# Kernel tuning notes

Measured on AMD Instinct MI355X. Metric: run time of the kernel, lower is better.

The kernel has to match this reference:

```python
import jax, jax.numpy as jnp
import numpy as np

APN, UEN, H, S = 105, 4000, 128, 10
BN_EPS = 1e-5


def _xavier(k, shape):
    fan_out, fan_in = shape
    return jax.random.normal(k, shape, dtype=jnp.float32) * jnp.sqrt(2.0 / (fan_in + fan_out))


def setup_inputs() -> dict:
    key = jax.random.key(0)
    ks = jax.random.split(key, 24)
    inp = {
        "pl": jax.random.normal(ks[0], (APN, UEN), dtype=jnp.float32),
        "require": jax.random.normal(ks[1], (UEN,), dtype=jnp.float32),
        "adj_ue": jax.random.randint(ks[2], (UEN, S), 0, APN, dtype=jnp.int32),
        "adj_ap": jax.random.randint(ks[3], (APN, S), 0, UEN, dtype=jnp.int32),
        # layer-1 Mean_layer weights [embed_dim, feature_dim]
        "W1_ap1": _xavier(ks[4], (H, UEN + APN)),
        "W1_ap2": _xavier(ks[5], (H, 2 * UEN)),
        "W1_ue1": _xavier(ks[6], (H, UEN + APN)),
        "W1_ue2": _xavier(ks[7], (H, 2 * APN)),
        # layer-2 Mean_layer weights
        "W2_ap1": _xavier(ks[8], (H, 4 * H)),
        "W2_ap2": _xavier(ks[9], (H, 4 * H)),
        "W2_ue1": _xavier(ks[10], (H, 4 * H)),
        "W2_ue2": _xavier(ks[11], (H, 4 * H)),
        # heads
        "weight_ap1": _xavier(ks[12], (2 * H, 2 * H)),
        "weight_ap2": _xavier(ks[13], (1, 2 * H)),
        "bais_ap": jax.random.uniform(ks[14], (APN,), dtype=jnp.float32),
        "weight_ue": _xavier(ks[15], (APN, 2 * H)),
        "bais_ue": jax.random.uniform(ks[16], (UEN,), dtype=jnp.float32),
        # BatchNorm1d affine params (training mode, batch stats)
        "bn_gamma": jnp.ones((2 * H,), dtype=jnp.float32),
        "bn_beta": jnp.zeros((2 * H,), dtype=jnp.float32),
    }
    return inp


def _agg(feats, idx):
    # GraphSage mean aggregate, exactly mask.sum/(num_neigh+1) of the original
    g = jnp.take(feats, idx, axis=0)            # [N, S, F]
    return g.sum(axis=1) / (idx.shape[1] + 1.0)  # [N, F]


def _two_hop(one_adj, sec_adj):
    # deterministic stand-in for union(sec_adj over one-hop) + sample(num_sample)
    s = one_adj.shape[1]
    g = jnp.take(sec_adj, one_adj, axis=0)       # [N, S, S]
    d = jnp.arange(s)
    return g[:, d, d]                            # [N, S]


def _layer(W, self_f, other_f, idx):
    comb = jnp.concatenate([self_f, _agg(other_f, idx)], axis=1)  # [N, feat]
    return jax.nn.relu(W @ comb.T)               # [H, N]


def _forward(pl, require, adj_ue, adj_ap, W1_ap1, W1_ap2, W1_ue1, W1_ue2,
             W2_ap1, W2_ap2, W2_ue1, W2_ue2, weight_ap1, weight_ap2,
             bais_ap, weight_ue, bais_ue, bn_gamma, bn_beta):
    feats_ap = pl            # [APN, UEN]
    feats_ue = pl.T          # [UEN, APN]

    ap2ap = _two_hop(adj_ap, adj_ue)   # AP -> AP 2-hop [APN, S]
    ue2ue = _two_hop(adj_ue, adj_ap)   # UE -> UE 2-hop [UEN, S]

    x1 = _layer(W1_ap1, feats_ap, feats_ue, adj_ap)   # [H, APN]
    x2 = _layer(W1_ap2, feats_ap, feats_ap, ap2ap)    # [H, APN]
    x3 = _layer(W1_ue1, feats_ue, feats_ap, adj_ue)   # [H, UEN]
    x4 = _layer(W1_ue2, feats_ue, feats_ue, ue2ue)    # [H, UEN]

    X_ap = jnp.concatenate([x1, x2], axis=0).T        # [APN, 2H]
    X_ue = jnp.concatenate([x3, x4], axis=0).T        # [UEN, 2H]

    x5 = _layer(W2_ap1, X_ap, X_ue, adj_ap)
    x6 = _layer(W2_ap2, X_ap, X_ap, ap2ap)
    x7 = _layer(W2_ue1, X_ue, X_ap, adj_ue)
    x8 = _layer(W2_ue2, X_ue, X_ue, ue2ue)

    X_ap2 = jnp.concatenate([x5, x6], axis=0)         # [2H, APN]
    hidden_pc = weight_ap1 @ X_ap2 + bais_ap          # [2H, APN] + [APN]
    PCoutcome = jax.nn.sigmoid((weight_ap2 @ hidden_pc).T)  # [APN, 1]

    X_ue2 = jnp.concatenate([x7, x8], axis=0)         # [2H, UEN]
    xt = X_ue2.T                                      # [UEN, 2H]
    mean = xt.mean(axis=0)
    var = xt.var(axis=0)                              # biased, training-mode BN
    xbn = ((xt - mean) / jnp.sqrt(var + BN_EPS)) * bn_gamma + bn_beta
    UA = weight_ue @ xbn.T + bais_ue                  # [APN, UEN] + [UEN]

    UA_ori = UA.T                                     # [UEN, APN]
    mx = UA_ori.max(axis=1, keepdims=True)
    mn = UA_ori.min(axis=1, keepdims=True)
    nor = (UA_ori - mx) / (mx - mn)
    UA_de = jax.nn.softmax(nor * 1000.0, axis=1)
    UA_st = jax.nn.softmax(nor, axis=1)
    var_ue = jnp.var(weight_ue, axis=1, ddof=1)       # torch.var unbiased
    return (UA_ori, UA_de, UA_st, PCoutcome, jnp.sum(var_ue))


def reference(pl, require, adj_ue, adj_ap, W1_ap1, W1_ap2, W1_ue1, W1_ue2,
              W2_ap1, W2_ap2, W2_ue1, W2_ue2, weight_ap1, weight_ap2,
              bais_ap, weight_ue, bais_ue, bn_gamma, bn_beta):
    return _forward(pl, require, adj_ue, adj_ap, W1_ap1, W1_ap2, W1_ue1,
                    W1_ue2, W2_ap1, W2_ap2, W2_ue1, W2_ue2, weight_ap1,
                    weight_ap2, bais_ap, weight_ue, bais_ue, bn_gamma, bn_beta)
```

## Files before the change

### kernel.cpp

```cpp
#include <hip/hip_runtime.h>
#include <math.h>
#include <float.h>


#define APN 105
#define UEN 4000
#define H   128
#define H2  256
#define SS  10
#define INV_NEIGH (1.0f/11.0f)
#define NKS 16
#define KSL 250
#define BNB 80

__device__ __forceinline__ float frelu(float v){ return v > 0.f ? v : 0.f; }

__global__ void k_twohop(const int* __restrict__ adj_ue, const int* __restrict__ adj_ap,
                         int* __restrict__ ap2ap, int* __restrict__ ue2ue){
  int idx = blockIdx.x*256 + threadIdx.x;
  if (idx >= (APN+UEN)*SS) return;
  if (idx < APN*SS){
    int s = idx % SS;
    ap2ap[idx] = adj_ue[adj_ap[idx]*SS + s];
  } else {
    int j = idx - APN*SS;
    int s = j % SS;
    ue2ue[j] = adj_ap[adj_ue[j]*SS + s];
  }
}

__device__ __forceinline__ void tile_core(const float (*As)[68], const float (*Bs)[68],
                                          int tx, int ty, float acc[4][4])
{
  #pragma unroll 4
  for (int k=0;k<32;k++){
    float a0 = As[k][ty*4+0], a1 = As[k][ty*4+1];
    float a2 = As[k][ty*4+2], a3 = As[k][ty*4+3];
    float b0 = Bs[k][tx*4+0], b1 = Bs[k][tx*4+1];
    float b2 = Bs[k][tx*4+2], b3 = Bs[k][tx*4+3];
    acc[0][0]=fmaf(a0,b0,acc[0][0]); acc[0][1]=fmaf(a0,b1,acc[0][1]);
    acc[0][2]=fmaf(a0,b2,acc[0][2]); acc[0][3]=fmaf(a0,b3,acc[0][3]);
    acc[1][0]=fmaf(a1,b0,acc[1][0]); acc[1][1]=fmaf(a1,b1,acc[1][1]);
    acc[1][2]=fmaf(a1,b2,acc[1][2]); acc[1][3]=fmaf(a1,b3,acc[1][3]);
    acc[2][0]=fmaf(a2,b0,acc[2][0]); acc[2][1]=fmaf(a2,b1,acc[2][1]);
    acc[2][2]=fmaf(a2,b2,acc[2][2]); acc[2][3]=fmaf(a2,b3,acc[2][3]);
    acc[3][0]=fmaf(a3,b0,acc[3][0]); acc[3][1]=fmaf(a3,b1,acc[3][1]);
    acc[3][2]=fmaf(a3,b2,acc[3][2]); acc[3][3]=fmaf(a3,b3,acc[3][3]);
  }
}

__global__ __launch_bounds__(256) void k_gemA6(
    const float* __restrict__ pl, const float* __restrict__ W1ap1,
    const float* __restrict__ W1ap2, const float* __restrict__ W1ue1,
    float* __restrict__ partial)
{
  __shared__ float As[32][68], Bs[32][68];
  int t = threadIdx.x;
  int n0 = blockIdx.x*64;
  int y = blockIdx.y;
  int ks = blockIdx.z;
  int slice = y>>1, h0 = (y&1)*64, k0 = ks*KSL;
  const float* w; int lda;
  if      (slice == 0){ w = W1ap1;       lda = UEN+APN; }
  else if (slice == 1){ w = W1ap2;       lda = 2*UEN;   }
  else if (slice == 2){ w = W1ap2 + UEN; lda = 2*UEN;   }
  else                { w = W1ue1 + APN; lda = UEN+APN; }
  int tx = t&15, ty = t>>4;
  int hr = t>>2, c0 = (t&3)*8;
  float acc[4][4] = {};
  for (int kc = 0; kc < 256; kc += 32){
    float w8[8], x8[8];
    const float* wr = w + (size_t)(h0+hr)*lda + k0 + kc + c0;
    #pragma unroll
    for (int i=0;i<8;i++) w8[i] = (kc+c0+i < KSL) ? wr[i] : 0.f;
    const float* xr = pl + (size_t)(n0+hr)*UEN + k0 + kc + c0;
    bool nok = (n0+hr < APN);
    #pragma unroll
    for (int i=0;i<8;i++) x8[i] = (nok && kc+c0+i < KSL) ? xr[i] : 0.f;
    __syncthreads();
    #pragma unroll
    for (int i=0;i<8;i++) As[c0+i][hr] = w8[i];
    #pragma unroll
    for (int i=0;i<8;i++) Bs[c0+i][hr] = x8[i];
    __syncthreads();
    tile_core(As, Bs, tx, ty, acc);
  }
  float* po = partial + (size_t)(slice*NKS+ks)*APN*H;
  #pragma unroll
  for (int j=0;j<4;j++){
    int n = n0 + tx*4 + j;
    if (n < APN){
      #pragma unroll
      for (int i=0;i<4;i++) po[(size_t)n*H + h0 + ty*4 + i] = acc[i][j];
    }
  }
}

__global__ __launch_bounds__(256) void k_redA(const float* __restrict__ partial,
                                              float* __restrict__ RA){
  int idx = blockIdx.x*256 + threadIdx.x;
  if (idx >= 4*APN*H) return;
  int slice = idx / (APN*H), r = idx % (APN*H);
  float s = 0.f;
  #pragma unroll
  for (int ks=0;ks<NKS;ks++) s += partial[((size_t)(slice*NKS+ks)*APN*H) + r];
  RA[idx] = s;
}

__global__ __launch_bounds__(256) void k_gemB2(
    const float* __restrict__ pl, const float* __restrict__ W1ap1,
    const float* __restrict__ W1ue1, const float* __restrict__ W1ue2,
    float* __restrict__ T3, float* __restrict__ T4,
    float* __restrict__ U1, float* __restrict__ R4)
{
  __shared__ float As[32][68], Bs[32][68];
  int t = threadIdx.x, u0 = blockIdx.x*64, y = blockIdx.y;
  int z = y>>1, h0 = (y&1)*64;
  const float* w; int lda; float* op;
  if      (z == 0){ w = W1ue1;       lda = UEN+APN; op = T3; }
  else if (z == 1){ w = W1ue2;       lda = 2*APN;   op = T4; }
  else if (z == 2){ w = W1ap1 + UEN; lda = UEN+APN; op = U1; }
  else            { w = W1ue2 + APN; lda = 2*APN;   op = R4; }
  int tx = t&15, ty = t>>4;
  int hr = t>>2,  c0 = (t&3)*8;
  int kr = t>>3, uu0 = (t&7)*8;
  float acc[4][4] = {};
  for (int kc=0; kc<128; kc+=32){
    float w8[8], x8[8];
    const float* wr = w + (size_t)(h0+hr)*lda + kc + c0;
    #pragma unroll
    for (int i=0;i<8;i++) w8[i] = (kc+c0+i < APN) ? wr[i] : 0.f;
    const float* xr = pl + (size_t)(kc+kr)*UEN + u0 + uu0;
    #pragma unroll
    for (int i=0;i<8;i++)
      x8[i] = (kc+kr < APN && u0+uu0+i < UEN) ? xr[i] : 0.f;
    __syncthreads();
    #pragma unroll
    for (int i=0;i<8;i++) As[c0+i][hr] = w8[i];
    #pragma unroll
    for (int i=0;i<8;i++) Bs[kr][uu0+i] = x8[i];
    __syncthreads();
    tile_core(As, Bs, tx, ty, acc);
  }
  #pragma unroll
  for (int j=0;j<4;j++){
    int u = u0 + tx*4 + j;
    if (u < UEN){
      #pragma unroll
      for (int i=0;i<4;i++) op[(size_t)u*H + h0 + ty*4 + i] = acc[i][j];
    }
  }
}

__global__ __launch_bounds__(256) void k_gemC2(
    const float* __restrict__ Xue, const float* __restrict__ W2ue1,
    const float* __restrict__ W2ue2, float* __restrict__ X2ue,
    float* __restrict__ Yb8)
{
  __shared__ float As[32][68], Bs[32][68];
  int t = threadIdx.x, u0 = blockIdx.x*64, y = blockIdx.y;
  int z = y>>1, h0 = (y&1)*64;
  const float* W = (z == 0) ? W2ue1 : W2ue2;
  int coff = (z == 2) ? H2 : 0;
  float* op; int ldo;
  if      (z == 0){ op = X2ue + h0;     ldo = H2; }
  else if (z == 1){ op = X2ue + H + h0; ldo = H2; }
  else            { op = Yb8 + h0;      ldo = H;  }
  int tx = t&15, ty = t>>4;
  int hr = t>>2, c0 = (t&3)*8;
  float acc[4][4] = {};
  for (int kc=0; kc<H2; kc+=32){
    float w8[8], x8[8];
    const float* wr = W + (size_t)(h0+hr)*(2*H2) + coff + kc + c0;
    #pragma unroll
    for (int i=0;i<8;i++) w8[i] = wr[i];
    const float* xr = Xue + (size_t)(u0+hr)*H2 + kc + c0;
    bool uok = (u0+hr < UEN);
    #pragma unroll
    for (int i=0;i<8;i++) x8[i] = uok ? xr[i] : 0.f;
    __syncthreads();
    #pragma unroll
    for (int i=0;i<8;i++) As[c0+i][hr] = w8[i];
    #pragma unroll
    for (int i=0;i<8;i++) Bs[c0+i][hr] = x8[i];
    __syncthreads();
    tile_core(As, Bs, tx, ty, acc);
  }
  #pragma unroll
  for (int j=0;j<4;j++){
    int u = u0 + tx*4 + j;
    if (u < UEN){
      #pragma unroll
      for (int i=0;i<4;i++) op[(size_t)u*ldo + ty*4 + i] = acc[i][j];
    }
  }
}

__global__ __launch_bounds__(256) void k_x_ueB(
    const float* __restrict__ T3, const float* __restrict__ T4,
    const float* __restrict__ P3t, const float* __restrict__ R4,
    const int* __restrict__ adj_ue, const int* __restrict__ ue2ue,
    float* __restrict__ Xue)
{
  __shared__ int aj[SS], u2[SS];
  int u = blockIdx.x, t = threadIdx.x;
  if (t < SS){ aj[t] = adj_ue[u*SS+t]; u2[t] = ue2ue[u*SS+t]; }
  __syncthreads();
  int h = t & (H-1);
  float g, s = 0.f;
  if (t < H){
    g = T3[(size_t)u*H + h];
    for (int q=0;q<SS;q++) s += P3t[(size_t)aj[q]*H + h];
  } else {
    g = T4[(size_t)u*H + h];
    for (int q=0;q<SS;q++) s += R4[(size_t)u2[q]*H + h];
  }
  Xue[(size_t)u*H2 + t] = frelu(g + s*INV_NEIGH);
}

__global__ __launch_bounds__(256) void k_x_ap(
    const float* __restrict__ RA, const float* __restrict__ U1,
    const int* __restrict__ adj_ap, const int* __restrict__ ap2ap,
    float* __restrict__ Xap)
{
  __shared__ int aj[SS], a2[SS];
  int i = blockIdx.x, t = threadIdx.x;
  if (t < SS){ aj[t] = adj_ap[i*SS+t]; a2[t] = ap2ap[i*SS+t]; }
  __syncthreads();
  int h = t & (H-1);
  float g, s = 0.f;
  if (t < H){
    g = RA[(size_t)i*H + h];
    for (int q=0;q<SS;q++) s += U1[(size_t)aj[q]*H + h];
  } else {
    g = RA[(size_t)APN*H + (size_t)i*H + h];
    const float* Q2t = RA + (size_t)2*APN*H;
    for (int q=0;q<SS;q++) s += Q2t[(size_t)a2[q]*H + h];
  }
  Xap[(size_t)i*H2 + t] = frelu(g + s*INV_NEIGH);
}

__global__ __launch_bounds__(128) void k_p7(
    const float* __restrict__ Xap, const float* __restrict__ W2ue1,
    float* __restrict__ P7t)
{
  __shared__ float xrow[H2];
  int n = blockIdx.x, t = threadIdx.x;
  xrow[t] = Xap[(size_t)n*H2 + t];
  xrow[t+128] = Xap[(size_t)n*H2 + t + 128];
  __syncthreads();
  const float* w = W2ue1 + (size_t)t*(2*H2) + H2;
  float s0=0.f,s1=0.f,s2=0.f,s3=0.f;
  for (int c=0;c<H2;c+=4){
    s0 = fmaf(w[c  ], xrow[c  ], s0);
    s1 = fmaf(w[c+1], xrow[c+1], s1);
    s2 = fmaf(w[c+2], xrow[c+2], s2);
    s3 = fmaf(w[c+3], xrow[c+3], s3);
  }
  P7t[(size_t)n*H + t] = (s0+s1)+(s2+s3);
}

__global__ __launch_bounds__(256) void k_x7x8b(
    float* __restrict__ X2ue, const float* __restrict__ P7t,
    const float* __restrict__ Yb8, const int* __restrict__ adj_ue,
    const int* __restrict__ ue2ue)
{
  __shared__ int aj[SS], u2[SS];
  int u = blockIdx.x, t = threadIdx.x;
  if (t < SS){ aj[t] = adj_ue[u*SS+t]; u2[t] = ue2ue[u*SS+t]; }
  __syncthreads();
  float g = X2ue[(size_t)u*H2 + t];
  float s = 0.f;
  if (t < H){
    for (int q=0;q<SS;q++) s += P7t[(size_t)aj[q]*H + t];
  } else {
    for (int q=0;q<SS;q++) s += Yb8[(size_t)u2[q]*H + (t-H)];
  }
  X2ue[(size_t)u*H2 + t] = frelu(g + s*INV_NEIGH);
}

__global__ __launch_bounds__(256) void k_ap_layer2_head(
    const float* __restrict__ Xap, const float* __restrict__ Xue,
    const float* __restrict__ W2ap1, const float* __restrict__ W2ap2,
    const int* __restrict__ adj_ap, const int* __restrict__ ap2ap,
    const float* __restrict__ wap1, const float* __restrict__ wap2,
    const float* __restrict__ bais_ap, float* __restrict__ out_pc)
{
  __shared__ float xa[H2], a5[H2], a6[H2], xs2[H2], red[256];
  __shared__ int aj[SS], a2i[SS];
  int i = blockIdx.x, t = threadIdx.x;
  if (t < SS){ aj[t] = adj_ap[i*SS+t]; a2i[t] = ap2ap[i*SS+t]; }
  __syncthreads();
  xa[t] = Xap[(size_t)i*H2+t];
  float s5=0.f, s6=0.f;
  for (int q=0;q<SS;q++){
    s5 += Xue[(size_t)aj[q]*H2 + t];
    s6 += Xap[(size_t)a2i[q]*H2 + t];
  }
  a5[t]=s5*INV_NEIGH; a6[t]=s6*INV_NEIGH;
  __syncthreads();
  const float* w; const float* agg;
  if (t < H){ w = W2ap1 + (size_t)t*(2*H2);     agg = a5; }
  else      { w = W2ap2 + (size_t)(t-H)*(2*H2); agg = a6; }
  float s0=0.f,s1=0.f,s2=0.f,s3=0.f;
  for (int c=0;c<H2;c+=4){
    s0 = fmaf(w[c  ], xa[c  ], s0);
    s1 = fmaf(w[c+1], xa[c+1], s1);
    s2 = fmaf(w[c+2], xa[c+2], s2);
    s3 = fmaf(w[c+3], xa[c+3], s3);
  }
  for (int c=0;c<H2;c+=4){
    s0 = fmaf(w[H2+c  ], agg[c  ], s0);
    s1 = fmaf(w[H2+c+1], agg[c+1], s1);
    s2 = fmaf(w[H2+c+2], agg[c+2], s2);
    s3 = fmaf(w[H2+c+3], agg[c+3], s3);
  }
  xs2[t] = frelu((s0+s1)+(s2+s3));
  __syncthreads();
  float hid = bais_ap[i];
  const float* wr1 = wap1 + (size_t)t*H2;
  for (int c=0;c<H2;c++) hid = fmaf(wr1[c], xs2[c], hid);
  red[t] = wap2[t]*hid;
  __syncthreads();
  for (int o=128;o>0;o>>=1){ if (t<o) red[t]+=red[t+o]; __syncthreads(); }
  if (t==0) out_pc[i] = 1.f/(1.f+expf(-red[0]));
}

__global__ __launch_bounds__(256) void k_bn_part(const float* __restrict__ X2ue,
                                                 float* __restrict__ part){
  int b = blockIdx.x, c = threadIdx.x;
  float s=0.f, s2=0.f;
  for (int u = b*50; u < (b+1)*50; u++){
    float v = X2ue[(size_t)u*H2 + c];
    s += v; s2 += v*v;
  }
  part[b*512 + c] = s;
  part[b*512 + 256 + c] = s2;
}

__global__ __launch_bounds__(256) void k_bn_final2(
    const float* __restrict__ part, const float* __restrict__ gamma,
    const float* __restrict__ beta, const float* __restrict__ wue,
    float* __restrict__ Wue_st, float* __restrict__ row_off,
    float* __restrict__ out_scalar)
{
  __shared__ float shs[H2], red[256];
  int t = threadIdx.x;
  float s=0.f, s2=0.f;
  for (int b=0;b<BNB;b++){ s += part[b*512+t]; s2 += part[b*512+256+t]; }
  float mean = s*(1.f/UEN);
  float var  = s2*(1.f/UEN) - mean*mean;
  float sc = gamma[t]*rsqrtf(var + 1e-5f);
  shs[t] = beta[t] - mean*sc;
  for (int a=0;a<APN;a++)
    Wue_st[(size_t)t*APN + a] = wue[(size_t)a*H2 + t]*sc;
  __syncthreads();
  float vsum = 0.f;
  if (t < APN){
    const float* wr = wue + (size_t)t*H2;
    float ro=0.f, S=0.f, S2=0.f;
    for (int c=0;c<H2;c++){
      float w = wr[c];
      ro = fmaf(w, shs[c], ro);
      S += w; S2 += w*w;
    }
    row_off[t] = ro;
    vsum = (S2 - S*S*(1.f/H2)) * (1.f/(H2-1));
  }
  red[t]=vsum; __syncthreads();
  for (int o=128;o>0;o>>=1){ if (t<o) red[t]+=red[t+o]; __syncthreads(); }
  if (t==0) out_scalar[0]=red[0];
}

__global__ __launch_bounds__(128) void k_ua_head2(
    const float* __restrict__ X2ue, const float* __restrict__ Wue_st,
    const float* __restrict__ row_off, const float* __restrict__ bais_ue,
    float* __restrict__ out)
{
  __shared__ float xs[8][H2];
  __shared__ float wmax[2], wmin[2], ws1[2], ws2[2];
  int u0 = blockIdx.x*8, t = threadIdx.x;
  #pragma unroll
  for (int q=0;q<8;q++){
    xs[q][t]     = X2ue[(size_t)(u0+q)*H2 + t];
    xs[q][t+128] = X2ue[(size_t)(u0+q)*H2 + t + 128];
  }
  __syncthreads();
  int a = t;
  float acc[8];
  #pragma unroll
  for (int q=0;q<8;q++) acc[q] = 0.f;
  if (a < APN){
    float ro = row_off[a];
    #pragma unroll
    for (int q=0;q<8;q++) acc[q] = ro + bais_ue[u0+q];
    for (int c=0;c<H2;c++){
      float w = Wue_st[(size_t)c*APN + a];
      #pragma unroll
      for (int q=0;q<8;q++) acc[q] = fmaf(w, xs[q][c], acc[q]);
    }
  }
  int wid = t>>6;
  for (int q=0;q<8;q++){
    float vmax = (a<APN) ? acc[q] : -FLT_MAX;
    float vmin = (a<APN) ? acc[q] :  FLT_MAX;
    #pragma unroll
    for (int o=32;o>0;o>>=1){
      vmax = fmaxf(vmax, __shfl_xor(vmax, o));
      vmin = fminf(vmin, __shfl_xor(vmin, o));
    }
    if ((t&63)==0){ wmax[wid]=vmax; wmin[wid]=vmin; }
    __syncthreads();
    float mx = fmaxf(wmax[0], wmax[1]);
    float mn = fminf(wmin[0], wmin[1]);
    float nor = (a<APN) ? (acc[q]-mx)/(mx-mn) : 0.f;
    float e1 = (a<APN) ? expf(nor*1000.f) : 0.f;
    float e2 = (a<APN) ? expf(nor)        : 0.f;
    float s1 = e1, s2 = e2;
    #pragma unroll
    for (int o=32;o>0;o>>=1){
      s1 += __shfl_xor(s1, o);
      s2 += __shfl_xor(s2, o);
    }
    if ((t&63)==0){ ws1[wid]=s1; ws2[wid]=s2; }
    __syncthreads();
    float S1 = ws1[0]+ws1[1], S2 = ws2[0]+ws2[1];
    if (a < APN){
      size_t u = u0+q;
      out[u*APN + a]                     = acc[q];
      out[(size_t)UEN*APN   + u*APN + a] = e1/S1;
      out[(size_t)2*UEN*APN + u*APN + a] = e2/S2;
    }
  }
}

extern "C" void kernel_launch(void* const* d_in, const int* in_sizes, int n_in,
                              void* d_out, int out_size, void* d_ws, size_t ws_size,
                              hipStream_t stream) {
  const float* pl      = (const float*)d_in[0];
  const int*   adj_ue  = (const int*)d_in[2];
  const int*   adj_ap  = (const int*)d_in[3];
  const float* W1ap1   = (const float*)d_in[4];
  const float* W1ap2   = (const float*)d_in[5];
  const float* W1ue1   = (const float*)d_in[6];
  const float* W1ue2   = (const float*)d_in[7];
  const float* W2ap1   = (const float*)d_in[8];
  const float* W2ap2   = (const float*)d_in[9];
  const float* W2ue1   = (const float*)d_in[10];
  const float* W2ue2   = (const float*)d_in[11];
  const float* wap1    = (const float*)d_in[12];
  const float* wap2    = (const float*)d_in[13];
  const float* bais_ap = (const float*)d_in[14];
  const float* wue     = (const float*)d_in[15];
  const float* bais_ue = (const float*)d_in[16];
  const float* gamma   = (const float*)d_in[17];
  const float* beta    = (const float*)d_in[18];
  float* out = (float*)d_out;
  (void)in_sizes; (void)n_in; (void)out_size; (void)ws_size;

  char* ws = (char*)d_ws;
  size_t off = 0;
  auto alloc = [&](size_t bytes)->char*{
    char* p = ws + off; off += (bytes + 255) & ~(size_t)255; return p;
  };
  int*   ap2ap  = (int*)alloc(APN*SS*4);
  int*   ue2ue  = (int*)alloc(UEN*SS*4);
  float* Xap    = (float*)alloc((size_t)APN*H2*4);
  float* Xue    = (float*)alloc((size_t)UEN*H2*4);
  float* X2ue   = (float*)alloc((size_t)UEN*H2*4);
  float* part   = (float*)alloc((size_t)BNB*512*4);
  float* Wue_st = (float*)alloc((size_t)H2*APN*4);
  float* rowoff = (float*)alloc(APN*4);
  float* partialA = Xue;
  float* T3 = X2ue;
  float* T4 = X2ue + 512000;
  float* U1  = out;
  float* Yb8 = out;
  float* R4  = out + 520000;
  float* RA  = out + 1040000;
  float* P3t = RA + (size_t)3*APN*H;
  float* P7t = out + 1100000;

  k_twohop        <<<dim3(((APN+UEN)*SS+255)/256), 256, 0, stream>>>(adj_ue, adj_ap, ap2ap, ue2ue);
  k_gemA6         <<<dim3(2,8,NKS), 256, 0, stream>>>(pl, W1ap1, W1ap2, W1ue1, partialA);
  k_redA          <<<dim3((4*APN*H+255)/256), 256, 0, stream>>>(partialA, RA);
  k_gemB2         <<<dim3((UEN+63)/64, 8), 256, 0, stream>>>(pl, W1ap1, W1ue1, W1ue2,
                                                             T3, T4, U1, R4);
  k_x_ueB         <<<dim3(UEN), 256, 0, stream>>>(T3, T4, P3t, R4, adj_ue, ue2ue, Xue);
  k_x_ap          <<<dim3(APN), 256, 0, stream>>>(RA, U1, adj_ap, ap2ap, Xap);
  k_p7            <<<dim3(APN), 128, 0, stream>>>(Xap, W2ue1, P7t);
  k_gemC2         <<<dim3((UEN+63)/64, 6), 256, 0, stream>>>(Xue, W2ue1, W2ue2, X2ue, Yb8);
  k_ap_layer2_head<<<dim3(APN), 256, 0, stream>>>(Xap, Xue, W2ap1, W2ap2, adj_ap, ap2ap,
                                                  wap1, wap2, bais_ap,
                                                  out + (size_t)3*UEN*APN);
  k_x7x8b         <<<dim3(UEN), 256, 0, stream>>>(X2ue, P7t, Yb8, adj_ue, ue2ue);
  k_bn_part       <<<dim3(BNB), 256, 0, stream>>>(X2ue, part);
  k_bn_final2     <<<dim3(1), 256, 0, stream>>>(part, gamma, beta, wue, Wue_st, rowoff,
                                                out + (size_t)3*UEN*APN + APN);
  k_ua_head2      <<<dim3(UEN/8), 128, 0, stream>>>(X2ue, Wue_st, rowoff, bais_ue, out);
}
```

Before: 268.5 us.

## Merge independent kernels into block-indexed mega-launches and fold BN finalize into head

Independent stages (two-hop index build, the two layer-1 GEMMs, weight-variance scalar) are merged into one launch that dispatches work by block index. The UE and AP aggregation kernels become one launch, and the layer-2 GEMM, P7 projection and AP head are packed into another. The single-block BN finalize is removed: each UA-head block now recomputes scale and shift from the partial sums and applies them to X2ue directly, reading wue row-major. This cuts the launch count from 13 to 7 and drops a serial one-block kernel, at the cost of redundant BN reduction work in every head block and heterogeneous blocks within each launch.

After: 220.2 us. 18.0% less time.

```diff
diff --git a/kernel.cpp b/kernel.cpp
--- a/kernel.cpp
+++ b/kernel.cpp
@@ -13,21 +13,12 @@
 #define KSL 250
 #define BNB 80
 
+#define NB_A 256
+#define NB_B 504
+#define NB_T 161
+#define NB_FRONT (NB_A+NB_B+NB_T+1)
+
 __device__ __forceinline__ float frelu(float v){ return v > 0.f ? v : 0.f; }
-
-__global__ void k_twohop(const int* __restrict__ adj_ue, const int* __restrict__ adj_ap,
-                         int* __restrict__ ap2ap, int* __restrict__ ue2ue){
-  int idx = blockIdx.x*256 + threadIdx.x;
-  if (idx >= (APN+UEN)*SS) return;
-  if (idx < APN*SS){
-    int s = idx % SS;
-    ap2ap[idx] = adj_ue[adj_ap[idx]*SS + s];
-  } else {
-    int j = idx - APN*SS;
-    int s = j % SS;
-    ue2ue[j] = adj_ap[adj_ue[j]*SS + s];
-  }
-}
 
 __device__ __forceinline__ void tile_core(const float (*As)[68], const float (*Bs)[68],
                                           int tx, int ty, float acc[4][4])
@@ -49,50 +40,119 @@
   }
 }
 
-__global__ __launch_bounds__(256) void k_gemA6(
+__global__ __launch_bounds__(256) void k_front(
     const float* __restrict__ pl, const float* __restrict__ W1ap1,
     const float* __restrict__ W1ap2, const float* __restrict__ W1ue1,
-    float* __restrict__ partial)
+    const float* __restrict__ W1ue2,
+    const int* __restrict__ adj_ue, const int* __restrict__ adj_ap,
+    int* __restrict__ ap2ap, int* __restrict__ ue2ue,
+    float* __restrict__ partial,
+    float* __restrict__ T3, float* __restrict__ T4,
+    float* __restrict__ U1, float* __restrict__ R4,
+    const float* __restrict__ wue, float* __restrict__ out_scalar)
 {
   __shared__ float As[32][68], Bs[32][68];
-  int t = threadIdx.x;
-  int n0 = blockIdx.x*64;
-  int y = blockIdx.y;
-  int ks = blockIdx.z;
-  int slice = y>>1, h0 = (y&1)*64, k0 = ks*KSL;
-  const float* w; int lda;
-  if      (slice == 0){ w = W1ap1;       lda = UEN+APN; }
-  else if (slice == 1){ w = W1ap2;       lda = 2*UEN;   }
-  else if (slice == 2){ w = W1ap2 + UEN; lda = 2*UEN;   }
-  else                { w = W1ue1 + APN; lda = UEN+APN; }
-  int tx = t&15, ty = t>>4;
-  int hr = t>>2, c0 = (t&3)*8;
-  float acc[4][4] = {};
-  for (int kc = 0; kc < 256; kc += 32){
-    float w8[8], x8[8];
-    const float* wr = w + (size_t)(h0+hr)*lda + k0 + kc + c0;
-    #pragma unroll
-    for (int i=0;i<8;i++) w8[i] = (kc+c0+i < KSL) ? wr[i] : 0.f;
-    const float* xr = pl + (size_t)(n0+hr)*UEN + k0 + kc + c0;
-    bool nok = (n0+hr < APN);
-    #pragma unroll
-    for (int i=0;i<8;i++) x8[i] = (nok && kc+c0+i < KSL) ? xr[i] : 0.f;
-    __syncthreads();
-    #pragma unroll
-    for (int i=0;i<8;i++) As[c0+i][hr] = w8[i];
-    #pragma unroll
-    for (int i=0;i<8;i++) Bs[c0+i][hr] = x8[i];
-    __syncthreads();
-    tile_core(As, Bs, tx, ty, acc);
-  }
-  float* po = partial + (size_t)(slice*NKS+ks)*APN*H;
-  #pragma unroll
-  for (int j=0;j<4;j++){
-    int n = n0 + tx*4 + j;
-    if (n < APN){
-      #pragma unroll
-      for (int i=0;i<4;i++) po[(size_t)n*H + h0 + ty*4 + i] = acc[i][j];
-    }
+  __shared__ float red[256];
+  int b = blockIdx.x, t = threadIdx.x;
+
+  if (b < NB_A){
+    int nt = b & 1, y = (b>>1) & 7, ks = b >> 4;
+    int n0 = nt*64, slice = y>>1, h0 = (y&1)*64, k0 = ks*KSL;
+    const float* w; int lda;
+    if      (slice == 0){ w = W1ap1;       lda = UEN+APN; }
+    else if (slice == 1){ w = W1ap2;       lda = 2*UEN;   }
+    else if (slice == 2){ w = W1ap2 + UEN; lda = 2*UEN;   }
+    else                { w = W1ue1 + APN; lda = UEN+APN; }
+    int tx = t&15, ty = t>>4;
+    int hr = t>>2, c0 = (t&3)*8;
+    float acc[4][4] = {};
+    for (int kc = 0; kc < 256; kc += 32){
+      float w8[8], x8[8];
+      const float* wr = w + (size_t)(h0+hr)*lda + k0 + kc + c0;
+      #pragma unroll
+      for (int i=0;i<8;i++) w8[i] = (kc+c0+i < KSL) ? wr[i] : 0.f;
+      const float* xr = pl + (size_t)(n0+hr)*UEN + k0 + kc + c0;
+      bool nok = (n0+hr < APN);
+      #pragma unroll
+      for (int i=0;i<8;i++) x8[i] = (nok && kc+c0+i < KSL) ? xr[i] : 0.f;
+      __syncthreads();
+      #pragma unroll
+      for (int i=0;i<8;i++) As[c0+i][hr] = w8[i];
+      #pragma unroll
+      for (int i=0;i<8;i++) Bs[c0+i][hr] = x8[i];
+      __syncthreads();
+      tile_core(As, Bs, tx, ty, acc);
+    }
+    float* po = partial + (size_t)(slice*NKS+ks)*APN*H;
+    #pragma unroll
+    for (int j=0;j<4;j++){
+      int n = n0 + tx*4 + j;
+      if (n < APN){
+        #pragma unroll
+        for (int i=0;i<4;i++) po[(size_t)n*H + h0 + ty*4 + i] = acc[i][j];
+      }
+    }
+  } else if (b < NB_A + NB_B){
+    int c = b - NB_A;
+    int u0 = (c % 63)*64, y = c / 63;
+    int z = y>>1, h0 = (y&1)*64;
+    const float* w; int lda; float* op;
+    if      (z == 0){ w = W1ue1;       lda = UEN+APN; op = T3; }
+    else if (z == 1){ w = W1ue2;       lda = 2*APN;   op = T4; }
+    else if (z == 2){ w = W1ap1 + UEN; lda = UEN+APN; op = U1; }
+    else            { w = W1ue2 + APN; lda = 2*APN;   op = R4; }
+    int tx = t&15, ty = t>>4;
+    int hr = t>>2,  c0 = (t&3)*8;
+    int kr = t>>3, uu0 = (t&7)*8;
+    float acc[4][4] = {};
+    for (int kc=0; kc<128; kc+=32){
+      float w8[8], x8[8];
+      const float* wr = w + (size_t)(h0+hr)*lda + kc + c0;
+      #pragma unroll
+      for (int i=0;i<8;i++) w8[i] = (kc+c0+i < APN) ? wr[i] : 0.f;
+      const float* xr = pl + (size_t)(kc+kr)*UEN + u0 + uu0;
+      #pragma unroll
+      for (int i=0;i<8;i++)
+        x8[i] = (kc+kr < APN && u0+uu0+i < UEN) ? xr[i] : 0.f;
+      __syncthreads();
+      #pragma unroll
+      for (int i=0;i<8;i++) As[c0+i][hr] = w8[i];
+      #pragma unroll
+      for (int i=0;i<8;i++) Bs[kr][uu0+i] = x8[i];
+      __syncthreads();
+      tile_core(As, Bs, tx, ty, acc);
+    }
+    #pragma unroll
+    for (int j=0;j<4;j++){
+      int u = u0 + tx*4 + j;
+      if (u < UEN){
+        #pragma unroll
+        for (int i=0;i<4;i++) op[(size_t)u*H + h0 + ty*4 + i] = acc[i][j];
+      }
+    }
+  } else if (b < NB_A + NB_B + NB_T){
+    int idx = (b - NB_A - NB_B)*256 + t;
+    if (idx < (APN+UEN)*SS){
+      if (idx < APN*SS){
+        int s = idx % SS;
+        ap2ap[idx] = adj_ue[adj_ap[idx]*SS + s];
+      } else {
+        int j = idx - APN*SS;
+        int s = j % SS;
+        ue2ue[j] = adj_ap[adj_ue[j]*SS + s];
+      }
+    }
+  } else {
+    float vsum = 0.f;
+    if (t < APN){
+      const float* wr = wue + (size_t)t*H2;
+      float S=0.f, S2=0.f;
+      for (int c=0;c<H2;c++){ float w=wr[c]; S+=w; S2+=w*w; }
+      vsum = (S2 - S*S*(1.f/H2)) * (1.f/(H2-1));
+    }
+    red[t]=vsum; __syncthreads();
+    for (int o=128;o>0;o>>=1){ if (t<o) red[t]+=red[t+o]; __syncthreads(); }
+    if (t==0) out_scalar[0]=red[0];
   }
 }
 
@@ -107,157 +167,152 @@
   RA[idx] = s;
 }
 
-__global__ __launch_bounds__(256) void k_gemB2(
-    const float* __restrict__ pl, const float* __restrict__ W1ap1,
-    const float* __restrict__ W1ue1, const float* __restrict__ W1ue2,
-    float* __restrict__ T3, float* __restrict__ T4,
-    float* __restrict__ U1, float* __restrict__ R4)
-{
-  __shared__ float As[32][68], Bs[32][68];
-  int t = threadIdx.x, u0 = blockIdx.x*64, y = blockIdx.y;
-  int z = y>>1, h0 = (y&1)*64;
-  const float* w; int lda; float* op;
-  if      (z == 0){ w = W1ue1;       lda = UEN+APN; op = T3; }
-  else if (z == 1){ w = W1ue2;       lda = 2*APN;   op = T4; }
-  else if (z == 2){ w = W1ap1 + UEN; lda = UEN+APN; op = U1; }
-  else            { w = W1ue2 + APN; lda = 2*APN;   op = R4; }
-  int tx = t&15, ty = t>>4;
-  int hr = t>>2,  c0 = (t&3)*8;
-  int kr = t>>3, uu0 = (t&7)*8;
-  float acc[4][4] = {};
-  for (int kc=0; kc<128; kc+=32){
-    float w8[8], x8[8];
-    const float* wr = w + (size_t)(h0+hr)*lda + kc + c0;
-    #pragma unroll
-    for (int i=0;i<8;i++) w8[i] = (kc+c0+i < APN) ? wr[i] : 0.f;
-    const float* xr = pl + (size_t)(kc+kr)*UEN + u0 + uu0;
-    #pragma unroll
-    for (int i=0;i<8;i++)
-      x8[i] = (kc+kr < APN && u0+uu0+i < UEN) ? xr[i] : 0.f;
-    __syncthreads();
-    #pragma unroll
-    for (int i=0;i<8;i++) As[c0+i][hr] = w8[i];
-    #pragma unroll
-    for (int i=0;i<8;i++) Bs[kr][uu0+i] = x8[i];
-    __syncthreads();
-    tile_core(As, Bs, tx, ty, acc);
-  }
-  #pragma unroll
-  for (int j=0;j<4;j++){
-    int u = u0 + tx*4 + j;
-    if (u < UEN){
-      #pragma unroll
-      for (int i=0;i<4;i++) op[(size_t)u*H + h0 + ty*4 + i] = acc[i][j];
-    }
-  }
-}
-
-__global__ __launch_bounds__(256) void k_gemC2(
-    const float* __restrict__ Xue, const float* __restrict__ W2ue1,
-    const float* __restrict__ W2ue2, float* __restrict__ X2ue,
-    float* __restrict__ Yb8)
-{
-  __shared__ float As[32][68], Bs[32][68];
-  int t = threadIdx.x, u0 = blockIdx.x*64, y = blockIdx.y;
-  int z = y>>1, h0 = (y&1)*64;
-  const float* W = (z == 0) ? W2ue1 : W2ue2;
-  int coff = (z == 2) ? H2 : 0;
-  float* op; int ldo;
-  if      (z == 0){ op = X2ue + h0;     ldo = H2; }
-  else if (z == 1){ op = X2ue + H + h0; ldo = H2; }
-  else            { op = Yb8 + h0;      ldo = H;  }
-  int tx = t&15, ty = t>>4;
-  int hr = t>>2, c0 = (t&3)*8;
-  float acc[4][4] = {};
-  for (int kc=0; kc<H2; kc+=32){
-    float w8[8], x8[8];
-    const float* wr = W + (size_t)(h0+hr)*(2*H2) + coff + kc + c0;
-    #pragma unroll
-    for (int i=0;i<8;i++) w8[i] = wr[i];
-    const float* xr = Xue + (size_t)(u0+hr)*H2 + kc + c0;
-    bool uok = (u0+hr < UEN);
-    #pragma unroll
-    for (int i=0;i<8;i++) x8[i] = uok ? xr[i] : 0.f;
-    __syncthreads();
-    #pragma unroll
-    for (int i=0;i<8;i++) As[c0+i][hr] = w8[i];
-    #pragma unroll
-    for (int i=0;i<8;i++) Bs[c0+i][hr] = x8[i];
-    __syncthreads();
-    tile_core(As, Bs, tx, ty, acc);
-  }
-  #pragma unroll
-  for (int j=0;j<4;j++){
-    int u = u0 + tx*4 + j;
-    if (u < UEN){
-      #pragma unroll
-      for (int i=0;i<4;i++) op[(size_t)u*ldo + ty*4 + i] = acc[i][j];
-    }
-  }
-}
-
-__global__ __launch_bounds__(256) void k_x_ueB(
+__global__ __launch_bounds__(256) void k_mid1(
     const float* __restrict__ T3, const float* __restrict__ T4,
     const float* __restrict__ P3t, const float* __restrict__ R4,
+    const float* __restrict__ RA, const float* __restrict__ U1,
     const int* __restrict__ adj_ue, const int* __restrict__ ue2ue,
-    float* __restrict__ Xue)
-{
-  __shared__ int aj[SS], u2[SS];
-  int u = blockIdx.x, t = threadIdx.x;
-  if (t < SS){ aj[t] = adj_ue[u*SS+t]; u2[t] = ue2ue[u*SS+t]; }
-  __syncthreads();
+    const int* __restrict__ adj_ap, const int* __restrict__ ap2ap,
+    float* __restrict__ Xue, float* __restrict__ Xap)
+{
+  __shared__ int aj[SS], b2[SS];
+  int b = blockIdx.x, t = threadIdx.x;
   int h = t & (H-1);
-  float g, s = 0.f;
-  if (t < H){
-    g = T3[(size_t)u*H + h];
-    for (int q=0;q<SS;q++) s += P3t[(size_t)aj[q]*H + h];
+  if (b < UEN){
+    int u = b;
+    if (t < SS){ aj[t] = adj_ue[u*SS+t]; b2[t] = ue2ue[u*SS+t]; }
+    __syncthreads();
+    float g, s = 0.f;
+    if (t < H){
+      g = T3[(size_t)u*H + h];
+      for (int q=0;q<SS;q++) s += P3t[(size_t)aj[q]*H + h];
+    } else {
+      g = T4[(size_t)u*H + h];
+      for (int q=0;q<SS;q++) s += R4[(size_t)b2[q]*H + h];
+    }
+    Xue[(size_t)u*H2 + t] = frelu(g + s*INV_NEIGH);
   } else {
-    g = T4[(size_t)u*H + h];
-    for (int q=0;q<SS;q++) s += R4[(size_t)u2[q]*H + h];
-  }
-  Xue[(size_t)u*H2 + t] = frelu(g + s*INV_NEIGH);
-}
-
-__global__ __launch_bounds__(256) void k_x_ap(
-    const float* __restrict__ RA, const float* __restrict__ U1,
+    int i = b - UEN;
+    if (t < SS){ aj[t] = adj_ap[i*SS+t]; b2[t] = ap2ap[i*SS+t]; }
+    __syncthreads();
+    float g, s = 0.f;
+    if (t < H){
+      g = RA[(size_t)i*H + h];
+      for (int q=0;q<SS;q++) s += U1[(size_t)aj[q]*H + h];
+    } else {
+      g = RA[(size_t)APN*H + (size_t)i*H + h];
+      const float* Q2t = RA + (size_t)2*APN*H;
+      for (int q=0;q<SS;q++) s += Q2t[(size_t)b2[q]*H + h];
+    }
+    Xap[(size_t)i*H2 + t] = frelu(g + s*INV_NEIGH);
+  }
+}
+
+__global__ __launch_bounds__(256) void k_mid2(
+    const float* __restrict__ Xue, const float* __restrict__ Xap,
+    const float* __restrict__ W2ue1, const float* __restrict__ W2ue2,
+    const float* __restrict__ W2ap1, const float* __restrict__ W2ap2,
     const int* __restrict__ adj_ap, const int* __restrict__ ap2ap,
-    float* __restrict__ Xap)
-{
-  __shared__ int aj[SS], a2[SS];
-  int i = blockIdx.x, t = threadIdx.x;
-  if (t < SS){ aj[t] = adj_ap[i*SS+t]; a2[t] = ap2ap[i*SS+t]; }
-  __syncthreads();
-  int h = t & (H-1);
-  float g, s = 0.f;
-  if (t < H){
-    g = RA[(size_t)i*H + h];
-    for (int q=0;q<SS;q++) s += U1[(size_t)aj[q]*H + h];
+    const float* __restrict__ wap1, const float* __restrict__ wap2,
+    const float* __restrict__ bais_ap,
+    float* __restrict__ X2ue, float* __restrict__ Yb8,
+    float* __restrict__ P7t, float* __restrict__ out_pc)
+{
+  __shared__ float As[32][68], Bs[32][68];
+  __shared__ float xa[H2], a5[H2], a6[H2], xs2[H2], red[256];
+  __shared__ int aj[SS], a2i[SS];
+  int b = blockIdx.x, t = threadIdx.x;
+
+  if (b < 378){
+    int u0 = (b % 63)*64, y = b / 63;
+    int z = y>>1, h0 = (y&1)*64;
+    const float* W = (z == 0) ? W2ue1 : W2ue2;
+    int coff = (z == 2) ? H2 : 0;
+    float* op; int ldo;
+    if      (z == 0){ op = X2ue + h0;     ldo = H2; }
+    else if (z == 1){ op = X2ue + H + h0; ldo = H2; }
+    else            { op = Yb8 + h0;      ldo = H;  }
+    int tx = t&15, ty = t>>4;
+    int hr = t>>2, c0 = (t&3)*8;
+    float acc[4][4] = {};
+    for (int kc=0; kc<H2; kc+=32){
+      float w8[8], x8[8];
+      const float* wr = W + (size_t)(h0+hr)*(2*H2) + coff + kc + c0;
+      #pragma unroll
+      for (int i=0;i<8;i++) w8[i] = wr[i];
+      const float* xr = Xue + (size_t)(u0+hr)*H2 + kc + c0;
+      bool uok = (u0+hr < UEN);
+      #pragma unroll
+      for (int i=0;i<8;i++) x8[i] = uok ? xr[i] : 0.f;
+      __syncthreads();
+      #pragma unroll
+      for (int i=0;i<8;i++) As[c0+i][hr] = w8[i];
+      #pragma unroll
+      for (int i=0;i<8;i++) Bs[c0+i][hr] = x8[i];
+      __syncthreads();
+      tile_core(As, Bs, tx, ty, acc);
+    }
+    #pragma unroll
+    for (int j=0;j<4;j++){
+      int u = u0 + tx*4 + j;
+      if (u < UEN){
+        #pragma unroll
+        for (int i=0;i<4;i++) op[(size_t)u*ldo + ty*4 + i] = acc[i][j];
+      }
+    }
+  } else if (b < 483){
+    int n = b - 378;
+    xa[t] = Xap[(size_t)n*H2 + t];
+    __syncthreads();
+    if (t < H){
+      const float* w = W2ue1 + (size_t)t*(2*H2) + H2;
+      float s0=0.f,s1=0.f,s2=0.f,s3=0.f;
+      for (int c=0;c<H2;c+=4){
+        s0 = fmaf(w[c  ], xa[c  ], s0);
+        s1 = fmaf(w[c+1], xa[c+1], s1);
+        s2 = fmaf(w[c+2], xa[c+2], s2);
+        s3 = fmaf(w[c+3], xa[c+3], s3);
+      }
+      P7t[(size_t)n*H + t] = (s0+s1)+(s2+s3);
+    }
   } else {
-    g = RA[(size_t)APN*H + (size_t)i*H + h];
-    const float* Q2t = RA + (size_t)2*APN*H;
-    for (int q=0;q<SS;q++) s += Q2t[(size_t)a2[q]*H + h];
-  }
-  Xap[(size_t)i*H2 + t] = frelu(g + s*INV_NEIGH);
-}
-
-__global__ __launch_bounds__(128) void k_p7(
-    const float* __restrict__ Xap, const float* __restrict__ W2ue1,
-    float* __restrict__ P7t)
-{
-  __shared__ float xrow[H2];
-  int n = blockIdx.x, t = threadIdx.x;
-  xrow[t] = Xap[(size_t)n*H2 + t];
-  xrow[t+128] = Xap[(size_t)n*H2 + t + 128];
-  __syncthreads();
-  const float* w = W2ue1 + (size_t)t*(2*H2) + H2;
-  float s0=0.f,s1=0.f,s2=0.f,s3=0.f;
-  for (int c=0;c<H2;c+=4){
-    s0 = fmaf(w[c  ], xrow[c  ], s0);
-    s1 = fmaf(w[c+1], xrow[c+1], s1);
-    s2 = fmaf(w[c+2], xrow[c+2], s2);
-    s3 = fmaf(w[c+3], xrow[c+3], s3);
-  }
-  P7t[(size_t)n*H + t] = (s0+s1)+(s2+s3);
+    int i = b - 483;
+    if (t < SS){ aj[t] = adj_ap[i*SS+t]; a2i[t] = ap2ap[i*SS+t]; }
+    __syncthreads();
+    xa[t] = Xap[(size_t)i*H2+t];
+    float s5=0.f, s6=0.f;
+    for (int q=0;q<SS;q++){
+      s5 += Xue[(size_t)aj[q]*H2 + t];
+      s6 += Xap[(size_t)a2i[q]*H2 + t];
+    }
+    a5[t]=s5*INV_NEIGH; a6[t]=s6*INV_NEIGH;
+    __syncthreads();
+    const float* w; const float* agg;
+    if (t < H){ w = W2ap1 + (size_t)t*(2*H2);     agg = a5; }
+    else      { w = W2ap2 + (size_t)(t-H)*(2*H2); agg = a6; }
+    float s0=0.f,s1=0.f,s2=0.f,s3=0.f;
+    for (int c=0;c<H2;c+=4){
+      s0 = fmaf(w[c  ], xa[c  ], s0);
+      s1 = fmaf(w[c+1], xa[c+1], s1);
+      s2 = fmaf(w[c+2], xa[c+2], s2);
+      s3 = fmaf(w[c+3], xa[c+3], s3);
+    }
+    for (int c=0;c<H2;c+=4){
+      s0 = fmaf(w[H2+c  ], agg[c  ], s0);
+      s1 = fmaf(w[H2+c+1], agg[c+1], s1);
+      s2 = fmaf(w[H2+c+2], agg[c+2], s2);
+      s3 = fmaf(w[H2+c+3], agg[c+3], s3);
+    }
+    xs2[t] = frelu((s0+s1)+(s2+s3));
+    __syncthreads();
+    float hid = bais_ap[i];
+    const float* wr1 = wap1 + (size_t)t*H2;
+    for (int c=0;c<H2;c++) hid = fmaf(wr1[c], xs2[c], hid);
+    red[t] = wap2[t]*hid;
+    __syncthreads();
+    for (int o=128;o>0;o>>=1){ if (t<o) red[t]+=red[t+o]; __syncthreads(); }
+    if (t==0) out_pc[i] = 1.f/(1.f+expf(-red[0]));
+  }
 }
 
 __global__ __launch_bounds__(256) void k_x7x8b(
@@ -279,53 +334,6 @@
   X2ue[(size_t)u*H2 + t] = frelu(g + s*INV_NEIGH);
 }
 
-__global__ __launch_bounds__(256) void k_ap_layer2_head(
-    const float* __restrict__ Xap, const float* __restrict__ Xue,
-    const float* __restrict__ W2ap1, const float* __restrict__ W2ap2,
-    const int* __restrict__ adj_ap, const int* __restrict__ ap2ap,
-    const float* __restrict__ wap1, const float* __restrict__ wap2,
-    const float* __restrict__ bais_ap, float* __restrict__ out_pc)
-{
-  __shared__ float xa[H2], a5[H2], a6[H2], xs2[H2], red[256];
-  __shared__ int aj[SS], a2i[SS];
-  int i = blockIdx.x, t = threadIdx.x;
-  if (t < SS){ aj[t] = adj_ap[i*SS+t]; a2i[t] = ap2ap[i*SS+t]; }
-  __syncthreads();
-  xa[t] = Xap[(size_t)i*H2+t];
-  float s5=0.f, s6=0.f;
-  for (int q=0;q<SS;q++){
-    s5 += Xue[(size_t)aj[q]*H2 + t];
-    s6 += Xap[(size_t)a2i[q]*H2 + t];
-  }
-  a5[t]=s5*INV_NEIGH; a6[t]=s6*INV_NEIGH;
-  __syncthreads();
-  const float* w; const float* agg;
-  if (t < H){ w = W2ap1 + (size_t)t*(2*H2);     agg = a5; }
-  else      { w = W2ap2 + (size_t)(t-H)*(2*H2); agg = a6; }
-  float s0=0.f,s1=0.f,s2=0.f,s3=0.f;
-  for (int c=0;c<H2;c+=4){
-    s0 = fmaf(w[c  ], xa[c  ], s0);
-    s1 = fmaf(w[c+1], xa[c+1], s1);
-    s2 = fmaf(w[c+2], xa[c+2], s2);
-    s3 = fmaf(w[c+3], xa[c+3], s3);
-  }
-  for (int c=0;c<H2;c+=4){
-    s0 = fmaf(w[H2+c  ], agg[c  ], s0);
-    s1 = fmaf(w[H2+c+1], agg[c+1], s1);
-    s2 = fmaf(w[H2+c+2], agg[c+2], s2);
-    s3 = fmaf(w[H2+c+3], agg[c+3], s3);
-  }
-  xs2[t] = frelu((s0+s1)+(s2+s3));
-  __syncthreads();
-  float hid = bais_ap[i];
-  const float* wr1 = wap1 + (size_t)t*H2;
-  for (int c=0;c<H2;c++) hid = fmaf(wr1[c], xs2[c], hid);
-  red[t] = wap2[t]*hid;
-  __syncthreads();
-  for (int o=128;o>0;o>>=1){ if (t<o) red[t]+=red[t+o]; __syncthreads(); }
-  if (t==0) out_pc[i] = 1.f/(1.f+expf(-red[0]));
-}
-
 __global__ __launch_bounds__(256) void k_bn_part(const float* __restrict__ X2ue,
                                                  float* __restrict__ part){
   int b = blockIdx.x, c = threadIdx.x;
@@ -338,52 +346,30 @@
   part[b*512 + 256 + c] = s2;
 }
 
-__global__ __launch_bounds__(256) void k_bn_final2(
-    const float* __restrict__ part, const float* __restrict__ gamma,
-    const float* __restrict__ beta, const float* __restrict__ wue,
-    float* __restrict__ Wue_st, float* __restrict__ row_off,
-    float* __restrict__ out_scalar)
-{
-  __shared__ float shs[H2], red[256];
-  int t = threadIdx.x;
-  float s=0.f, s2=0.f;
-  for (int b=0;b<BNB;b++){ s += part[b*512+t]; s2 += part[b*512+256+t]; }
-  float mean = s*(1.f/UEN);
-  float var  = s2*(1.f/UEN) - mean*mean;
-  float sc = gamma[t]*rsqrtf(var + 1e-5f);
-  shs[t] = beta[t] - mean*sc;
-  for (int a=0;a<APN;a++)
-    Wue_st[(size_t)t*APN + a] = wue[(size_t)a*H2 + t]*sc;
-  __syncthreads();
-  float vsum = 0.f;
-  if (t < APN){
-    const float* wr = wue + (size_t)t*H2;
-    float ro=0.f, S=0.f, S2=0.f;
-    for (int c=0;c<H2;c++){
-      float w = wr[c];
-      ro = fmaf(w, shs[c], ro);
-      S += w; S2 += w*w;
-    }
-    row_off[t] = ro;
-    vsum = (S2 - S*S*(1.f/H2)) * (1.f/(H2-1));
-  }
-  red[t]=vsum; __syncthreads();
-  for (int o=128;o>0;o>>=1){ if (t<o) red[t]+=red[t+o]; __syncthreads(); }
-  if (t==0) out_scalar[0]=red[0];
-}
-
-__global__ __launch_bounds__(128) void k_ua_head2(
-    const float* __restrict__ X2ue, const float* __restrict__ Wue_st,
-    const float* __restrict__ row_off, const float* __restrict__ bais_ue,
+__global__ __launch_bounds__(128) void k_ua_head3(
+    const float* __restrict__ X2ue, const float* __restrict__ part,
+    const float* __restrict__ gamma, const float* __restrict__ beta,
+    const float* __restrict__ wue, const float* __restrict__ bais_ue,
     float* __restrict__ out)
 {
   __shared__ float xs[8][H2];
+  __shared__ float scs[H2], shs[H2];
   __shared__ float wmax[2], wmin[2], ws1[2], ws2[2];
   int u0 = blockIdx.x*8, t = threadIdx.x;
+  for (int c = t; c < H2; c += 128){
+    float s=0.f, s2=0.f;
+    for (int b=0;b<BNB;b++){ s += part[b*512+c]; s2 += part[b*512+256+c]; }
+    float mean = s*(1.f/UEN);
+    float var  = s2*(1.f/UEN) - mean*mean;
+    float sc = gamma[c]*rsqrtf(var + 1e-5f);
+    scs[c] = sc;
+    shs[c] = beta[c] - mean*sc;
+  }
+  __syncthreads();
   #pragma unroll
   for (int q=0;q<8;q++){
-    xs[q][t]     = X2ue[(size_t)(u0+q)*H2 + t];
-    xs[q][t+128] = X2ue[(size_t)(u0+q)*H2 + t + 128];
+    xs[q][t]     = X2ue[(size_t)(u0+q)*H2 + t]*scs[t] + shs[t];
+    xs[q][t+128] = X2ue[(size_t)(u0+q)*H2 + t + 128]*scs[t+128] + shs[t+128];
   }
   __syncthreads();
   int a = t;
@@ -391,11 +377,11 @@
   #pragma unroll
   for (int q=0;q<8;q++) acc[q] = 0.f;
   if (a < APN){
-    float ro = row_off[a];
-    #pragma unroll
-    for (int q=0;q<8;q++) acc[q] = ro + bais_ue[u0+q];
+    #pragma unroll
+    for (int q=0;q<8;q++) acc[q] = bais_ue[u0+q];
+    const float* wr = wue + (size_t)a*H2;
     for (int c=0;c<H2;c++){
-      float w = Wue_st[(size_t)c*APN + a];
+      float w = wr[c];
       #pragma unroll
       for (int q=0;q<8;q++) acc[q] = fmaf(w, xs[q][c], acc[q]);
     }
@@ -469,8 +455,6 @@
   float* Xue    = (float*)alloc((size_t)UEN*H2*4);
   float* X2ue   = (float*)alloc((size_t)UEN*H2*4);
   float* part   = (float*)alloc((size_t)BNB*512*4);
-  float* Wue_st = (float*)alloc((size_t)H2*APN*4);
-  float* rowoff = (float*)alloc(APN*4);
   float* partialA = Xue;
   float* T3 = X2ue;
   float* T4 = X2ue + 512000;
@@ -480,22 +464,22 @@
   float* RA  = out + 1040000;
   float* P3t = RA + (size_t)3*APN*H;
   float* P7t = out + 1100000;
-
-  k_twohop        <<<dim3(((APN+UEN)*SS+255)/256), 256, 0, stream>>>(adj_ue, adj_ap, ap2ap, ue2ue);
-  k_gemA6         <<<dim3(2,8,NKS), 256, 0, stream>>>(pl, W1ap1, W1ap2, W1ue1, partialA);
-  k_redA          <<<dim3((4*APN*H+255)/256), 256, 0, stream>>>(partialA, RA);
-  k_gemB2         <<<dim3((UEN+63)/64, 8), 256, 0, stream>>>(pl, W1ap1, W1ue1, W1ue2,
-                                                             T3, T4, U1, R4);
-  k_x_ueB         <<<dim3(UEN), 256, 0, stream>>>(T3, T4, P3t, R4, adj_ue, ue2ue, Xue);
-  k_x_ap          <<<dim3(APN), 256, 0, stream>>>(RA, U1, adj_ap, ap2ap, Xap);
-  k_p7            <<<dim3(APN), 128, 0, stream>>>(Xap, W2ue1, P7t);
-  k_gemC2         <<<dim3((UEN+63)/64, 6), 256, 0, stream>>>(Xue, W2ue1, W2ue2, X2ue, Yb8);
-  k_ap_layer2_head<<<dim3(APN), 256, 0, stream>>>(Xap, Xue, W2ap1, W2ap2, adj_ap, ap2ap,
-                                                  wap1, wap2, bais_ap,
-                                                  out + (size_t)3*UEN*APN);
-  k_x7x8b         <<<dim3(UEN), 256, 0, stream>>>(X2ue, P7t, Yb8, adj_ue, ue2ue);
-  k_bn_part       <<<dim3(BNB), 256, 0, stream>>>(X2ue, part);
-  k_bn_final2     <<<dim3(1), 256, 0, stream>>>(part, gamma, beta, wue, Wue_st, rowoff,
-                                                out + (size_t)3*UEN*APN + APN);
-  k_ua_head2      <<<dim3(UEN/8), 128, 0, stream>>>(X2ue, Wue_st, rowoff, bais_ue, out);
-}
+  float* out_pc = out + (size_t)3*UEN*APN;
+  float* out_sc = out + (size_t)3*UEN*APN + APN;
+
+  k_front   <<<dim3(NB_FRONT), 256, 0, stream>>>(pl, W1ap1, W1ap2, W1ue1, W1ue2,
+                                                 adj_ue, adj_ap, ap2ap, ue2ue,
+                                                 partialA, T3, T4, U1, R4,
+                                                 wue, out_sc);
+  k_redA    <<<dim3((4*APN*H+255)/256), 256, 0, stream>>>(partialA, RA);
+  k_mid1    <<<dim3(UEN+APN), 256, 0, stream>>>(T3, T4, P3t, R4, RA, U1,
+                                                adj_ue, ue2ue, adj_ap, ap2ap,
+                                                Xue, Xap);
+  k_mid2    <<<dim3(588), 256, 0, stream>>>(Xue, Xap, W2ue1, W2ue2, W2ap1, W2ap2,
+                                            adj_ap, ap2ap, wap1, wap2, bais_ap,
+                                            X2ue, Yb8, P7t, out_pc);
+  k_x7x8b   <<<dim3(UEN), 256, 0, stream>>>(X2ue, P7t, Yb8, adj_ue, ue2ue);
+  k_bn_part <<<dim3(BNB), 256, 0, stream>>>(X2ue, part);
+  k_ua_head3<<<dim3(UEN/8), 128, 0, stream>>>(X2ue, part, gamma, beta, wue,
+                                              bais_ue, out);
+}
```
